# Performance work log

Hardware: AMD Instinct MI355X
Metric: run time of the kernel (lower is better)

Reference implementation:

```python
import jax, jax.numpy as jnp
import numpy as np

NUM_HEADS = 12

def _pe(L, d):
    # standard sinusoidal positional encoding, shape (1, L, d)
    pos = jnp.arange(L, dtype=jnp.float32)[:, None]
    i = jnp.arange(d)[None, :]
    angle = pos / jnp.power(10000.0, (2 * (i // 2)).astype(jnp.float32) / d)
    pe = jnp.where(i % 2 == 0, jnp.sin(angle), jnp.cos(angle))
    return pe[None]

def _ln(x, scale, bias, eps=1e-5):
    m = x.mean(-1, keepdims=True)
    v = ((x - m) ** 2).mean(-1, keepdims=True)
    return (x - m) / jnp.sqrt(v + eps) * scale + bias

def setup_inputs() -> dict:
    key = jax.random.key(0)
    ks = jax.random.split(key, 8)
    D = 768
    s = 0.02
    return {
        "x": jax.random.normal(ks[0], (8, D, 32, 32), jnp.float32),
        "context_token": jax.random.normal(ks[1], (1, 1, D), jnp.float32),
        "register_tokens": jax.random.normal(ks[2], (1, 4, D), jnp.float32),
        "in_proj_w": jax.random.normal(ks[3], (3 * D, D), jnp.float32) * s,
        "in_proj_b": jnp.zeros((3 * D,), jnp.float32),
        "out_proj_w": jax.random.normal(ks[4], (D, D), jnp.float32) * s,
        "out_proj_b": jnp.zeros((D,), jnp.float32),
        "ln1_s": jnp.ones((D,), jnp.float32),
        "ln1_b": jnp.zeros((D,), jnp.float32),
        "ln2_s": jnp.ones((D,), jnp.float32),
        "ln2_b": jnp.zeros((D,), jnp.float32),
        "ffn_w1": jax.random.normal(ks[5], (4 * D, D), jnp.float32) * s,
        "ffn_b1": jnp.zeros((4 * D,), jnp.float32),
        "ffn_w2": jax.random.normal(ks[6], (D, 4 * D), jnp.float32) * s,
        "ffn_b2": jnp.zeros((D,), jnp.float32),
    }

def reference(x, context_token, register_tokens, in_proj_w, in_proj_b,
              out_proj_w, out_proj_b, ln1_s, ln1_b, ln2_s, ln2_b,
              ffn_w1, ffn_b1, ffn_w2, ffn_b2):
    B, d, h, w = x.shape
    N = h * w
    R = register_tokens.shape[1]
    G = 1 + R  # global tokens: context + registers
    nh = NUM_HEADS
    dh = d // nh
    # (B, N, d)
    x_flat = x.reshape(B, d, N).transpose(0, 2, 1)
    tokens = jnp.concatenate([
        jnp.broadcast_to(context_token, (B, 1, d)),
        jnp.broadcast_to(register_tokens, (B, R, d)),
    ], axis=1)
    tokens = tokens + _pe(G, d)
    xwt = _ln(jnp.concatenate([tokens, x_flat], axis=1), ln1_s, ln1_b)
    S = G + N
    # MultiheadAttention (eval mode, dropout off): fused in-projection
    qkv = xwt @ in_proj_w.T + in_proj_b
    q, k, v = jnp.split(qkv, 3, axis=-1)
    to_heads = lambda t: t.reshape(B, S, nh, dh).transpose(0, 2, 1, 3)
    q, k, v = to_heads(q), to_heads(k), to_heads(v)
    scores = jnp.einsum('bhqd,bhkd->bhqk', q, k) / np.float32(np.sqrt(dh))
    # mask (True = disallowed): feature rows (>=G) cannot attend to global cols (<G);
    # global rows attend everything; feature-feature block allowed.
    row_feat = jnp.arange(S) >= G
    col_glob = jnp.arange(S) < G
    disallowed = row_feat[:, None] & col_glob[None, :]
    scores = jnp.where(disallowed, -jnp.inf, scores)
    attn = jax.nn.softmax(scores, axis=-1)
    o = jnp.einsum('bhqk,bhkd->bhqd', attn, v).transpose(0, 2, 1, 3).reshape(B, S, d)
    o = o @ out_proj_w.T + out_proj_b
    y = o + xwt
    ff = jax.nn.gelu(_ln(y, ln2_s, ln2_b) @ ffn_w1.T + ffn_b1, approximate=False) @ ffn_w2.T + ffn_b2
    y = y + ff
    context_out = y[:, 0:1, :]
    register_out = y[:, 1:G, :]
    feature_out = y[:, G:, :].transpose(0, 2, 1).reshape(B, d, h, w)
    return feature_out, context_out, register_out
```

## Files before the change

### kernel.cpp

```cpp
#include <hip/hip_runtime.h>
#include <hip/hip_bf16.h>
#include <cmath>

typedef unsigned short u16;
typedef __bf16 bf16x8 __attribute__((ext_vector_type(8)));
typedef float floatx4 __attribute__((ext_vector_type(4)));

#define SQ 1029
#define DM 768
#define NH 12
#define SQP 1088

#define GLD16(gp, lp) __builtin_amdgcn_global_load_lds( \
    (const __attribute__((address_space(1))) unsigned int*)(gp), \
    (__attribute__((address_space(3))) unsigned int*)(lp), 16, 0, 0)

#define OFF_WQKV ((size_t)0)
#define OFF_WOUT ((size_t)3538944)
#define OFF_W1   ((size_t)4718592)
#define OFF_W2   ((size_t)9437184)
#define OFF_XF   ((size_t)14155776)
#define OFF_XWT  ((size_t)26800128)
#define OFF_Q    ((size_t)39444480)
#define OFF_K    ((size_t)52813824)
#define OFF_V    ((size_t)66183168)
#define OFF_VT   ((size_t)79552512)
#define OFF_Y    ((size_t)92921856)

__device__ __forceinline__ float bf2f(u16 u) {
  unsigned int x = ((unsigned int)u) << 16;
  float f; __builtin_memcpy(&f, &x, 4); return f;
}
__device__ __forceinline__ u16 f2bf(float f) {
  unsigned int x; __builtin_memcpy(&x, &x, 0);
  __builtin_memcpy(&x, &f, 4);
  x = (x + 0x7fffu + ((x >> 16) & 1u)) >> 16;
  return (u16)x;
}
__device__ __forceinline__ unsigned int pk_bf16(float a, float b) {
  __hip_bfloat162 h = __float22bfloat162_rn(make_float2(a, b));
  unsigned int u; __builtin_memcpy(&u, &h, 4); return u;
}

__device__ __forceinline__ void blockReduce2(float& s1, float& s2) {
  #pragma unroll
  for (int o = 32; o > 0; o >>= 1) { s1 += __shfl_xor(s1, o); s2 += __shfl_xor(s2, o); }
  __shared__ float t1[4], t2[4];
  const int w = threadIdx.x >> 6;
  if ((threadIdx.x & 63) == 0) { t1[w] = s1; t2[w] = s2; }
  __syncthreads();
  s1 = t1[0] + t1[1] + t1[2] + t1[3];
  s2 = t2[0] + t2[1] + t2[2] + t2[3];
}

__global__ __launch_bounds__(256) void convw_all(
    const float* __restrict__ a, const float* __restrict__ b,
    const float* __restrict__ c, const float* __restrict__ d, u16* __restrict__ dst) {
  int i = blockIdx.x * 256 + threadIdx.x;
  if (i >= 1769472) return;
  const float* src; int off;
  if (i < 442368)       { src = a; off = i; }
  else if (i < 589824)  { src = b; off = i - 442368; }
  else if (i < 1179648) { src = c; off = i - 589824; }
  else                  { src = d; off = i - 1179648; }
  float4 v = ((const float4*)src)[off];
  ushort4 o; o.x = f2bf(v.x); o.y = f2bf(v.y); o.z = f2bf(v.z); o.w = f2bf(v.w);
  ((ushort4*)dst)[i] = o;
}

__global__ __launch_bounds__(256) void transpose_x(const float* __restrict__ x, u16* __restrict__ xf) {
  __shared__ u16 tile[32][33];
  const int b = blockIdx.x, ct = blockIdx.y, nt = blockIdx.z;
  const int i = threadIdx.x, jj = threadIdx.y;
  #pragma unroll
  for (int kk = 0; kk < 4; ++kk) {
    int j = jj + kk * 8;
    tile[j][i] = f2bf(x[((size_t)b * 768 + ct * 32 + j) * 1024 + nt * 32 + i]);
  }
  __syncthreads();
  #pragma unroll
  for (int kk = 0; kk < 4; ++kk) {
    int j = jj + kk * 8;
    xf[((size_t)b * 1024 + nt * 32 + j) * 768 + ct * 32 + i] = tile[i][j];
  }
}

__global__ __launch_bounds__(256) void build_xwt(
    const u16* __restrict__ xf, const float* __restrict__ ctx, const float* __restrict__ regt,
    const float* __restrict__ g, const float* __restrict__ be, u16* __restrict__ xwt) {
  const int row = blockIdx.x;
  const int b = row / SQ, s = row % SQ;
  const int tid = threadIdx.x;
  float v[3];
  #pragma unroll
  for (int i = 0; i < 3; ++i) {
    const int c = tid + i * 256;
    float val;
    if (s >= 5) {
      val = bf2f(xf[((size_t)b * 1024 + (s - 5)) * DM + c]);
    } else {
      float tok = (s == 0) ? ctx[c] : regt[(s - 1) * DM + c];
      float e = (float)(2 * (c / 2)) * (1.0f / 768.0f);
      float ang = (float)s / powf(10000.0f, e);
      val = tok + ((c & 1) ? cosf(ang) : sinf(ang));
    }
    v[i] = val;
  }
  float s1 = v[0] + v[1] + v[2];
  float s2 = v[0] * v[0] + v[1] * v[1] + v[2] * v[2];
  blockReduce2(s1, s2);
  const float mean = s1 * (1.0f / 768.0f);
  const float var = s2 * (1.0f / 768.0f) - mean * mean;
  const float rs = rsqrtf(fmaxf(var, 0.0f) + 1e-5f);
  #pragma unroll
  for (int i = 0; i < 3; ++i) {
    const int c = tid + i * 256;
    xwt[(size_t)row * DM + c] = f2bf((v[i] - mean) * rs * g[c] + be[c]);
  }
}

__global__ __launch_bounds__(256) void ln2k(
    const u16* __restrict__ y, const float* __restrict__ g, const float* __restrict__ be,
    u16* __restrict__ out) {
  const int row = blockIdx.x;
  const int tid = threadIdx.x;
  float v[3];
  #pragma unroll
  for (int i = 0; i < 3; ++i) v[i] = bf2f(y[(size_t)row * DM + tid + i * 256]);
  float s1 = v[0] + v[1] + v[2];
  float s2 = v[0] * v[0] + v[1] * v[1] + v[2] * v[2];
  blockReduce2(s1, s2);
  const float mean = s1 * (1.0f / 768.0f);
  const float var = s2 * (1.0f / 768.0f) - mean * mean;
  const float rs = rsqrtf(fmaxf(var, 0.0f) + 1e-5f);
  #pragma unroll
  for (int i = 0; i < 3; ++i) {
    const int c = tid + i * 256;
    out[(size_t)row * DM + c] = f2bf((v[i] - mean) * rs * g[c] + be[c]);
  }
}

template<int EPI>
__global__ __launch_bounds__(256) void gemm128(
    const u16* __restrict__ A, const u16* __restrict__ W, const float* __restrict__ bias,
    void* __restrict__ p0, void* __restrict__ p1, void* __restrict__ p2,
    int M, int N, int K) {
  __shared__ u16 As[8192];
  __shared__ u16 Bs[8192];
  const int tid = threadIdx.x, wave = tid >> 6, lane = tid & 63, quad = lane >> 4, l16 = lane & 15;
  const int m0 = blockIdx.x * 128, n0 = blockIdx.y * 128;
  const int wm = wave & 1, wn = wave >> 1;

  const u16* Ap[4]; const u16* Wp[4]; u16* la[4]; u16* lb[4];
  #pragma unroll
  for (int it = 0; it < 4; ++it) {
    const int c = it * 256 + tid;
    const int row = c >> 3, gch = (c & 7) ^ (row & 7);
    Ap[it] = A + (size_t)min(m0 + row, M - 1) * K + gch * 8;
    Wp[it] = W + (size_t)(n0 + row) * K + gch * 8;
    la[it] = As + it * 2048 + wave * 512;
    lb[it] = Bs + it * 2048 + wave * 512;
  }

  floatx4 acc[4][4];
  #pragma unroll
  for (int i = 0; i < 4; ++i)
    #pragma unroll
    for (int j = 0; j < 4; ++j) { floatx4 z = {0.f, 0.f, 0.f, 0.f}; acc[i][j] = z; }

  for (int k0 = 0; k0 < K; k0 += 64) {
    __syncthreads();
    #pragma unroll
    for (int it = 0; it < 4; ++it) GLD16(Ap[it] + k0, la[it]);
    #pragma unroll
    for (int it = 0; it < 4; ++it) GLD16(Wp[it] + k0, lb[it]);
    __syncthreads();
    #pragma unroll
    for (int kk = 0; kk < 2; ++kk) {
      bf16x8 a[4], b[4];
      const int ch = ((kk * 4 + quad) ^ (l16 & 7)) << 3;
      #pragma unroll
      for (int i = 0; i < 4; ++i) a[i] = *(const bf16x8*)&As[(wm * 64 + i * 16 + l16) * 64 + ch];
      #pragma unroll
      for (int j = 0; j < 4; ++j) b[j] = *(const bf16x8*)&Bs[(wn * 64 + j * 16 + l16) * 64 + ch];
      #pragma unroll
      for (int i = 0; i < 4; ++i)
        #pragma unroll
        for (int j = 0; j < 4; ++j)
          acc[i][j] = __builtin_amdgcn_mfma_f32_16x16x32_bf16(a[i], b[j], acc[i][j], 0, 0, 0);
    }
  }

  if constexpr (EPI == 0) {
    const int sec = n0 / 768;
    u16* dst = (sec == 0) ? (u16*)p0 : (sec == 1) ? (u16*)p1 : (u16*)p2;
    #pragma unroll
    for (int i = 0; i < 4; ++i) {
      #pragma unroll
      for (int r = 0; r < 4; ++r) {
        const int row = m0 + wm * 64 + i * 16 + quad * 4 + r;
        if (row >= M) continue;
        const int bb = row / SQ, ss = row - bb * SQ;
        #pragma unroll
        for (int j = 0; j < 4; ++j) {
          const int cc = n0 + wn * 64 + j * 16 + l16;
          const int hh = (cc - sec * 768) >> 6;
          const int dh = cc & 63;
          dst[(((size_t)bb * NH + hh) * SQP + ss) * 64 + dh] = f2bf(acc[i][j][r] + bias[cc]);
        }
      }
    }
  } else {
    #pragma unroll
    for (int i = 0; i < 4; ++i) {
      #pragma unroll
      for (int r = 0; r < 4; ++r) {
        const int row = m0 + wm * 64 + i * 16 + quad * 4 + r;
        if (row >= M) continue;
        #pragma unroll
        for (int j = 0; j < 4; ++j) {
          const int cc = n0 + wn * 64 + j * 16 + l16;
          const size_t idx = (size_t)row * N + cc;
          float v = acc[i][j][r] + bias[cc];
          if constexpr (EPI == 1) {
            v += bf2f(((const u16*)p1)[idx]);
            ((u16*)p0)[idx] = f2bf(v);
          } else if constexpr (EPI == 2) {
            v = v / (1.0f + exp2f(-2.3022221f * (v + 0.044715f * v * v * v)));
            ((u16*)p0)[idx] = f2bf(v);
          } else {
            v += bf2f(((const u16*)p1)[idx]);
            ((float*)p0)[idx] = v;
          }
        }
      }
    }
  }
}

__global__ __launch_bounds__(256) void vtrans(const u16* __restrict__ v, u16* __restrict__ vt) {
  __shared__ u16 t[32][33];
  const int bh = blockIdx.x, st = blockIdx.y, dt = blockIdx.z;
  const u16* vs = v + (size_t)bh * SQP * 64;
  u16* vd = vt + (size_t)bh * 64 * SQP;
  const int i = threadIdx.x, jj = threadIdx.y;
  #pragma unroll
  for (int kk = 0; kk < 4; ++kk) {
    int j = jj + kk * 8;
    t[j][i] = vs[(size_t)(st * 32 + j) * 64 + dt * 32 + i];
  }
  __syncthreads();
  #pragma unroll
  for (int kk = 0; kk < 4; ++kk) {
    int j = jj + kk * 8;
    vd[(size_t)(dt * 32 + j) * SQP + st * 32 + i] = t[i][j];
  }
}

__global__ __launch_bounds__(256) void attn_flash(
    const u16* __restrict__ q, const u16* __restrict__ k, const u16* __restrict__ vt,
    u16* __restrict__ out) {
  const int bh = blockIdx.x, qt = blockIdx.y;
  const int b = bh / NH, h = bh % NH;
  const int tid = threadIdx.x, wave = tid >> 6, lane = tid & 63, quad = lane >> 4, l16 = lane & 15;
  __shared__ u16 Qs[4096], Ks[4096], VTs[4096];
  __shared__ u16 Ps[64 * 72];
  const int q0 = qt * 64;
  const u16* qslab = q + (size_t)bh * SQP * 64;
  const u16* kslab = k + (size_t)bh * SQP * 64;
  const u16* vslab = vt + (size_t)bh * 64 * SQP;
  const int c0 = tid, c1 = tid + 256;
  const int r0 = c0 >> 3, q0c = (c0 & 7) ^ (r0 & 7);
  const int r1 = c1 >> 3, q1c = (c1 & 7) ^ (r1 & 7);
  const int g0 = r0 * 64 + q0c * 8;
  const int g1 = r1 * 64 + q1c * 8;
  u16* L0Q = Qs + wave * 512;  u16* L1Q = Qs + 2048 + wave * 512;
  u16* L0K = Ks + wave * 512;  u16* L1K = Ks + 2048 + wave * 512;
  u16* L0V = VTs + wave * 512; u16* L1V = VTs + 2048 + wave * 512;

  GLD16(qslab + q0 * 64 + g0, L0Q);
  GLD16(qslab + q0 * 64 + g1, L1Q);

  floatx4 Oa[4];
  #pragma unroll
  for (int nt = 0; nt < 4; ++nt) { floatx4 z = {0.f, 0.f, 0.f, 0.f}; Oa[nt] = z; }
  float l_acc = 0.f;
  const int qrow = wave * 16 + l16;
  const int qg = q0 + qrow;
  const bool qfeat = (qg >= 5);
  const float ssc = 0.125f * 1.44269504088896f;

  for (int t = 0; t < 17; ++t) {
    const int k0 = t * 64;
    __syncthreads();
    GLD16(kslab + k0 * 64 + g0, L0K);
    GLD16(kslab + k0 * 64 + g1, L1K);
    GLD16(vslab + (size_t)r0 * SQP + k0 + q0c * 8, L0V);
    GLD16(vslab + (size_t)r1 * SQP + k0 + q1c * 8, L1V);
    __syncthreads();

    floatx4 st[4];
    #pragma unroll
    for (int mt = 0; mt < 4; ++mt) { floatx4 z = {0.f, 0.f, 0.f, 0.f}; st[mt] = z; }
    #pragma unroll
    for (int kk = 0; kk < 2; ++kk) {
      bf16x8 qf = *(const bf16x8*)&Qs[qrow * 64 + (((kk * 4 + quad) ^ (qrow & 7)) << 3)];
      #pragma unroll
      for (int mt = 0; mt < 4; ++mt) {
        const int krow = mt * 16 + l16;
        bf16x8 kf = *(const bf16x8*)&Ks[krow * 64 + (((kk * 4 + quad) ^ (krow & 7)) << 3)];
        st[mt] = __builtin_amdgcn_mfma_f32_16x16x32_bf16(kf, qf, st[mt], 0, 0, 0);
      }
    }

    #pragma unroll
    for (int mt = 0; mt < 4; ++mt) {
      float p[4];
      #pragma unroll
      for (int r = 0; r < 4; ++r) {
        const int kg = k0 + mt * 16 + quad * 4 + r;
        const bool masked = (kg >= SQ) || (qfeat && kg < 5);
        float pv = exp2f(st[mt][r] * ssc);
        pv = masked ? 0.f : pv;
        p[r] = pv;
        l_acc += pv;
      }
      uint2 w;
      w.x = pk_bf16(p[0], p[1]);
      w.y = pk_bf16(p[2], p[3]);
      *(uint2*)&Ps[qrow * 72 + mt * 16 + quad * 4] = w;
    }

    #pragma unroll
    for (int kk = 0; kk < 2; ++kk) {
      bf16x8 pf = *(const bf16x8*)&Ps[qrow * 72 + kk * 32 + quad * 8];
      #pragma unroll
      for (int nt = 0; nt < 4; ++nt) {
        const int brow = nt * 16 + l16;
        bf16x8 bb = *(const bf16x8*)&VTs[brow * 64 + (((kk * 4 + quad) ^ (brow & 7)) << 3)];
        Oa[nt] = __builtin_amdgcn_mfma_f32_16x16x32_bf16(pf, bb, Oa[nt], 0, 0, 0);
      }
    }
  }

  float lt = l_acc;
  lt += __shfl_xor(lt, 16);
  lt += __shfl_xor(lt, 32);
  lt = fmaxf(lt, 1e-30f);
  #pragma unroll
  for (int nt = 0; nt < 4; ++nt)
    #pragma unroll
    for (int r = 0; r < 4; ++r) {
      const int qo = quad * 4 + r;
      const float lr = __shfl(lt, (lane & 48) | qo);
      const int qg2 = q0 + wave * 16 + qo;
      if (qg2 < SQ)
        out[((size_t)b * SQ + qg2) * DM + h * 64 + nt * 16 + l16] = f2bf(Oa[nt][r] / lr);
    }
}

__global__ __launch_bounds__(256) void transpose_out(const float* __restrict__ yf, float* __restrict__ out) {
  __shared__ float tile[32][33];
  const int b = blockIdx.x, nt = blockIdx.y, ct = blockIdx.z;
  const int i = threadIdx.x, jj = threadIdx.y;
  #pragma unroll
  for (int kk = 0; kk < 4; ++kk) {
    int j = jj + kk * 8;
    tile[j][i] = yf[((size_t)b * SQ + 5 + nt * 32 + j) * DM + ct * 32 + i];
  }
  __syncthreads();
  #pragma unroll
  for (int kk = 0; kk < 4; ++kk) {
    int j = jj + kk * 8;
    out[((size_t)b * 768 + ct * 32 + j) * 1024 + nt * 32 + i] = tile[i][j];
  }
}

__global__ __launch_bounds__(256) void out_small(const float* __restrict__ yf, float* __restrict__ out) {
  const int idx = blockIdx.x * 256 + threadIdx.x;
  if (idx >= 8 * 5 * DM) return;
  const int b = idx / (5 * DM);
  const int r = idx % (5 * DM);
  const int s = r / DM, c = r % DM;
  const float v = yf[((size_t)b * SQ + s) * DM + c];
  if (s == 0) out[(size_t)6291456 + (size_t)b * DM + c] = v;
  else out[(size_t)6291456 + 6144 + ((size_t)b * 4 + (s - 1)) * DM + c] = v;
}

extern "C" void kernel_launch(void* const* d_in, const int* in_sizes, int n_in,
                              void* d_out, int out_size, void* d_ws, size_t ws_size,
                              hipStream_t stream) {
  const float* x    = (const float*)d_in[0];
  const float* ctx  = (const float*)d_in[1];
  const float* regt = (const float*)d_in[2];
  const float* wqkv = (const float*)d_in[3];
  const float* bqkv = (const float*)d_in[4];
  const float* wout = (const float*)d_in[5];
  const float* bout = (const float*)d_in[6];
  const float* ln1s = (const float*)d_in[7];
  const float* ln1b = (const float*)d_in[8];
  const float* ln2s = (const float*)d_in[9];
  const float* ln2b = (const float*)d_in[10];
  const float* w1   = (const float*)d_in[11];
  const float* b1   = (const float*)d_in[12];
  const float* w2   = (const float*)d_in[13];
  const float* b2   = (const float*)d_in[14];

  char* ws = (char*)d_ws;
  u16* wb_all = (u16*)(ws + OFF_WQKV);
  u16* wqkv_b = (u16*)(ws + OFF_WQKV);
  u16* wout_b = (u16*)(ws + OFF_WOUT);
  u16* w1_b   = (u16*)(ws + OFF_W1);
  u16* w2_b   = (u16*)(ws + OFF_W2);
  u16* xf     = (u16*)(ws + OFF_XF);
  u16* xwt    = (u16*)(ws + OFF_XWT);
  u16* qb     = (u16*)(ws + OFF_Q);
  u16* kb     = (u16*)(ws + OFF_K);
  u16* vb     = (u16*)(ws + OFF_V);
  u16* vtb    = (u16*)(ws + OFF_VT);
  u16* yb     = (u16*)(ws + OFF_Y);
  u16* attnb  = (u16*)(ws + OFF_XF);
  u16* ynorm  = (u16*)(ws + OFF_XF);
  u16* h1     = (u16*)(ws + OFF_Q);
  float* yfin = (float*)(ws + OFF_XF);
  float* outp = (float*)d_out;

  convw_all   <<<6912, 256, 0, stream>>>(wqkv, wout, w1, w2, wb_all);
  transpose_x <<<dim3(8, 24, 32), dim3(32, 8), 0, stream>>>(x, xf);
  build_xwt   <<<8232, 256, 0, stream>>>(xf, ctx, regt, ln1s, ln1b, xwt);
  gemm128<0>  <<<dim3(65, 18), 256, 0, stream>>>(xwt, wqkv_b, bqkv, qb, kb, vb, 8232, 2304, 768);
  vtrans      <<<dim3(96, 34, 2), dim3(32, 8), 0, stream>>>(vb, vtb);
  attn_flash  <<<dim3(96, 17), 256, 0, stream>>>(qb, kb, vtb, attnb);
  gemm128<1>  <<<dim3(65, 6), 256, 0, stream>>>(attnb, wout_b, bout, yb, xwt, nullptr, 8232, 768, 768);
  ln2k        <<<8232, 256, 0, stream>>>(yb, ln2s, ln2b, ynorm);
  gemm128<2>  <<<dim3(65, 24), 256, 0, stream>>>(ynorm, w1_b, b1, h1, nullptr, nullptr, 8232, 3072, 768);
  gemm128<3>  <<<dim3(65, 6), 256, 0, stream>>>(h1, w2_b, b2, yfin, yb, nullptr, 8232, 768, 3072);
  transpose_out<<<dim3(8, 32, 24), dim3(32, 8), 0, stream>>>(yfin, outp);
  out_small   <<<120, 256, 0, stream>>>(yfin, outp);
}
```

Baseline: 464.4 us.

## Template GEMM on K/N, add grouped block swizzle, vectorized LDS-staged epilogue, fused QKV layout

The GEMM becomes a templated kernel with compile-time K and N. It adds a grouped 1D block order so that eight M-tiles share each weight tile, and swaps the MFMA operands so each lane holds four consecutive columns. The epilogue stages results through shared memory and writes 16-byte coalesced bf16 stores with a vectorized residual add. The QKV projection now writes a single row-major [S,2304] buffer that attention and vtrans read with strided loads, and the final output is kept in bf16 instead of fp32. This cuts scattered 2-byte stores and output traffic, at the cost of less-coalesced Q/K loads in attention and an extra rounding of the final output to bf16.

```diff
diff --git a/kernel.cpp b/kernel.cpp
--- a/kernel.cpp
+++ b/kernel.cpp
@@ -21,19 +21,16 @@
 #define OFF_W2   ((size_t)9437184)
 #define OFF_XF   ((size_t)14155776)
 #define OFF_XWT  ((size_t)26800128)
-#define OFF_Q    ((size_t)39444480)
-#define OFF_K    ((size_t)52813824)
-#define OFF_V    ((size_t)66183168)
-#define OFF_VT   ((size_t)79552512)
-#define OFF_Y    ((size_t)92921856)
+#define OFF_QKV  ((size_t)39444480)
+#define OFF_VT   ((size_t)77783040)
+#define OFF_Y    ((size_t)91152384)
 
 __device__ __forceinline__ float bf2f(u16 u) {
   unsigned int x = ((unsigned int)u) << 16;
   float f; __builtin_memcpy(&f, &x, 4); return f;
 }
 __device__ __forceinline__ u16 f2bf(float f) {
-  unsigned int x; __builtin_memcpy(&x, &x, 0);
-  __builtin_memcpy(&x, &f, 4);
+  unsigned int x; __builtin_memcpy(&x, &f, 4);
   x = (x + 0x7fffu + ((x >> 16) & 1u)) >> 16;
   return (u16)x;
 }
@@ -140,15 +137,21 @@
   }
 }
 
-template<int EPI>
-__global__ __launch_bounds__(256) void gemm128(
+template<int EPI, int K, int NB>
+__global__ __launch_bounds__(256) void gemmk(
     const u16* __restrict__ A, const u16* __restrict__ W, const float* __restrict__ bias,
-    void* __restrict__ p0, void* __restrict__ p1, void* __restrict__ p2,
-    int M, int N, int K) {
-  __shared__ u16 As[8192];
-  __shared__ u16 Bs[8192];
+    const u16* __restrict__ res, u16* __restrict__ out, int M) {
+  constexpr int N = NB * 128;
+  __shared__ u16 SM[16384];
+  u16* Asm = SM;
+  u16* Bsm = SM + 8192;
   const int tid = threadIdx.x, wave = tid >> 6, lane = tid & 63, quad = lane >> 4, l16 = lane & 15;
-  const int m0 = blockIdx.x * 128, n0 = blockIdx.y * 128;
+  const int lin = blockIdx.x;
+  constexpr int FULL = 64 * NB;
+  int mb, nb;
+  if (lin < FULL) { const int g = lin / (8 * NB); const int r = lin - g * 8 * NB; mb = g * 8 + (r & 7); nb = r >> 3; }
+  else { mb = 64; nb = lin - FULL; }
+  const int m0 = mb * 128, n0 = nb * 128;
   const int wm = wave & 1, wn = wave >> 1;
 
   const u16* Ap[4]; const u16* Wp[4]; u16* la[4]; u16* lb[4];
@@ -158,8 +161,8 @@
     const int row = c >> 3, gch = (c & 7) ^ (row & 7);
     Ap[it] = A + (size_t)min(m0 + row, M - 1) * K + gch * 8;
     Wp[it] = W + (size_t)(n0 + row) * K + gch * 8;
-    la[it] = As + it * 2048 + wave * 512;
-    lb[it] = Bs + it * 2048 + wave * 512;
+    la[it] = Asm + c * 8;
+    lb[it] = Bsm + c * 8;
   }
 
   floatx4 acc[4][4];
@@ -168,86 +171,107 @@
     #pragma unroll
     for (int j = 0; j < 4; ++j) { floatx4 z = {0.f, 0.f, 0.f, 0.f}; acc[i][j] = z; }
 
-  for (int k0 = 0; k0 < K; k0 += 64) {
-    __syncthreads();
-    #pragma unroll
-    for (int it = 0; it < 4; ++it) GLD16(Ap[it] + k0, la[it]);
-    #pragma unroll
-    for (int it = 0; it < 4; ++it) GLD16(Wp[it] + k0, lb[it]);
-    __syncthreads();
-    #pragma unroll
-    for (int kk = 0; kk < 2; ++kk) {
-      bf16x8 a[4], b[4];
-      const int ch = ((kk * 4 + quad) ^ (l16 & 7)) << 3;
-      #pragma unroll
-      for (int i = 0; i < 4; ++i) a[i] = *(const bf16x8*)&As[(wm * 64 + i * 16 + l16) * 64 + ch];
-      #pragma unroll
-      for (int j = 0; j < 4; ++j) b[j] = *(const bf16x8*)&Bs[(wn * 64 + j * 16 + l16) * 64 + ch];
-      #pragma unroll
-      for (int i = 0; i < 4; ++i)
+  const int ch0 = (quad ^ (l16 & 7)) << 3;
+  const int ch1 = ((4 + quad) ^ (l16 & 7)) << 3;
+
+  #pragma unroll 1
+  for (int ko = 0; ko < K / 768; ++ko) {
+    #pragma unroll
+    for (int ki = 0; ki < 768; ki += 64) {
+      __syncthreads();
+      #pragma unroll
+      for (int it = 0; it < 4; ++it) GLD16(Ap[it] + ki, la[it]);
+      #pragma unroll
+      for (int it = 0; it < 4; ++it) GLD16(Wp[it] + ki, lb[it]);
+      __syncthreads();
+      #pragma unroll
+      for (int kk = 0; kk < 2; ++kk) {
+        const int ch = kk ? ch1 : ch0;
+        bf16x8 a[4], b[4];
         #pragma unroll
-        for (int j = 0; j < 4; ++j)
-          acc[i][j] = __builtin_amdgcn_mfma_f32_16x16x32_bf16(a[i], b[j], acc[i][j], 0, 0, 0);
-    }
-  }
-
-  if constexpr (EPI == 0) {
-    const int sec = n0 / 768;
-    u16* dst = (sec == 0) ? (u16*)p0 : (sec == 1) ? (u16*)p1 : (u16*)p2;
+        for (int i = 0; i < 4; ++i) a[i] = *(const bf16x8*)&Asm[(wm * 64 + i * 16 + l16) * 64 + ch];
+        #pragma unroll
+        for (int j = 0; j < 4; ++j) b[j] = *(const bf16x8*)&Bsm[(wn * 64 + j * 16 + l16) * 64 + ch];
+        #pragma unroll
+        for (int i = 0; i < 4; ++i)
+          #pragma unroll
+          for (int j = 0; j < 4; ++j)
+            acc[i][j] = __builtin_amdgcn_mfma_f32_16x16x32_bf16(b[j], a[i], acc[i][j], 0, 0, 0);
+      }
+    }
+    if (K > 768) {
+      #pragma unroll
+      for (int it = 0; it < 4; ++it) { Ap[it] += 768; Wp[it] += 768; }
+    }
+  }
+
+  #pragma unroll
+  for (int j = 0; j < 4; ++j) {
+    const float4 b4 = *(const float4*)(bias + n0 + wn * 64 + j * 16 + quad * 4);
     #pragma unroll
     for (int i = 0; i < 4; ++i) {
-      #pragma unroll
-      for (int r = 0; r < 4; ++r) {
-        const int row = m0 + wm * 64 + i * 16 + quad * 4 + r;
-        if (row >= M) continue;
-        const int bb = row / SQ, ss = row - bb * SQ;
+      acc[i][j][0] += b4.x; acc[i][j][1] += b4.y; acc[i][j][2] += b4.z; acc[i][j][3] += b4.w;
+    }
+  }
+  if constexpr (EPI == 2) {
+    #pragma unroll
+    for (int i = 0; i < 4; ++i)
+      #pragma unroll
+      for (int j = 0; j < 4; ++j)
         #pragma unroll
-        for (int j = 0; j < 4; ++j) {
-          const int cc = n0 + wn * 64 + j * 16 + l16;
-          const int hh = (cc - sec * 768) >> 6;
-          const int dh = cc & 63;
-          dst[(((size_t)bb * NH + hh) * SQP + ss) * 64 + dh] = f2bf(acc[i][j][r] + bias[cc]);
+        for (int r = 0; r < 4; ++r) {
+          const float v = acc[i][j][r];
+          acc[i][j][r] = v / (1.0f + exp2f(-2.3022221f * (v + 0.044715f * v * v * v)));
         }
-      }
-    }
-  } else {
-    #pragma unroll
-    for (int i = 0; i < 4; ++i) {
-      #pragma unroll
-      for (int r = 0; r < 4; ++r) {
-        const int row = m0 + wm * 64 + i * 16 + quad * 4 + r;
-        if (row >= M) continue;
+  }
+  __syncthreads();
+  u16* Ep = SM + wave * 2304;
+  #pragma unroll
+  for (int h = 0; h < 2; ++h) {
+    #pragma unroll
+    for (int i2 = 0; i2 < 2; ++i2) {
+      const int i = h * 2 + i2;
+      #pragma unroll
+      for (int j = 0; j < 4; ++j) {
+        uint2 w;
+        w.x = pk_bf16(acc[i][j][0], acc[i][j][1]);
+        w.y = pk_bf16(acc[i][j][2], acc[i][j][3]);
+        *(uint2*)&Ep[(i2 * 16 + l16) * 72 + j * 16 + quad * 4] = w;
+      }
+    }
+    #pragma unroll
+    for (int s = 0; s < 4; ++s) {
+      const int lrow = s * 8 + (lane >> 3);
+      const int gm = m0 + wm * 64 + h * 32 + lrow;
+      const int gn = n0 + wn * 64 + (lane & 7) * 8;
+      uint4 lv = *(const uint4*)&Ep[lrow * 72 + (lane & 7) * 8];
+      if constexpr (EPI == 1 || EPI == 3) {
+        const uint4 rv = *(const uint4*)(res + (size_t)min(gm, M - 1) * N + gn);
+        const unsigned* lp = &lv.x; const unsigned* rp = &rv.x;
+        uint4 ov; unsigned* op = &ov.x;
         #pragma unroll
-        for (int j = 0; j < 4; ++j) {
-          const int cc = n0 + wn * 64 + j * 16 + l16;
-          const size_t idx = (size_t)row * N + cc;
-          float v = acc[i][j][r] + bias[cc];
-          if constexpr (EPI == 1) {
-            v += bf2f(((const u16*)p1)[idx]);
-            ((u16*)p0)[idx] = f2bf(v);
-          } else if constexpr (EPI == 2) {
-            v = v / (1.0f + exp2f(-2.3022221f * (v + 0.044715f * v * v * v)));
-            ((u16*)p0)[idx] = f2bf(v);
-          } else {
-            v += bf2f(((const u16*)p1)[idx]);
-            ((float*)p0)[idx] = v;
-          }
+        for (int d = 0; d < 4; ++d) {
+          const float a0 = bf2f((u16)(lp[d] & 0xffffu)) + bf2f((u16)(rp[d] & 0xffffu));
+          const float a1 = bf2f((u16)(lp[d] >> 16)) + bf2f((u16)(rp[d] >> 16));
+          op[d] = pk_bf16(a0, a1);
         }
-      }
-    }
-  }
-}
-
-__global__ __launch_bounds__(256) void vtrans(const u16* __restrict__ v, u16* __restrict__ vt) {
+        lv = ov;
+      }
+      if (gm < M) *(uint4*)(out + (size_t)gm * N + gn) = lv;
+    }
+  }
+}
+
+__global__ __launch_bounds__(256) void vtrans(const u16* __restrict__ qkv, u16* __restrict__ vt) {
   __shared__ u16 t[32][33];
   const int bh = blockIdx.x, st = blockIdx.y, dt = blockIdx.z;
-  const u16* vs = v + (size_t)bh * SQP * 64;
+  const int bq = bh / NH, hh = bh % NH;
   u16* vd = vt + (size_t)bh * 64 * SQP;
   const int i = threadIdx.x, jj = threadIdx.y;
   #pragma unroll
   for (int kk = 0; kk < 4; ++kk) {
     int j = jj + kk * 8;
-    t[j][i] = vs[(size_t)(st * 32 + j) * 64 + dt * 32 + i];
+    t[j][i] = qkv[(size_t)(bq * SQ + st * 32 + j) * 2304 + 1536 + hh * 64 + dt * 32 + i];
   }
   __syncthreads();
   #pragma unroll
@@ -258,28 +282,24 @@
 }
 
 __global__ __launch_bounds__(256) void attn_flash(
-    const u16* __restrict__ q, const u16* __restrict__ k, const u16* __restrict__ vt,
-    u16* __restrict__ out) {
+    const u16* __restrict__ qkv, const u16* __restrict__ vt, u16* __restrict__ out) {
   const int bh = blockIdx.x, qt = blockIdx.y;
   const int b = bh / NH, h = bh % NH;
   const int tid = threadIdx.x, wave = tid >> 6, lane = tid & 63, quad = lane >> 4, l16 = lane & 15;
   __shared__ u16 Qs[4096], Ks[4096], VTs[4096];
   __shared__ u16 Ps[64 * 72];
   const int q0 = qt * 64;
-  const u16* qslab = q + (size_t)bh * SQP * 64;
-  const u16* kslab = k + (size_t)bh * SQP * 64;
+  const u16* qk = qkv + (size_t)b * SQ * 2304 + h * 64;
   const u16* vslab = vt + (size_t)bh * 64 * SQP;
   const int c0 = tid, c1 = tid + 256;
   const int r0 = c0 >> 3, q0c = (c0 & 7) ^ (r0 & 7);
   const int r1 = c1 >> 3, q1c = (c1 & 7) ^ (r1 & 7);
-  const int g0 = r0 * 64 + q0c * 8;
-  const int g1 = r1 * 64 + q1c * 8;
   u16* L0Q = Qs + wave * 512;  u16* L1Q = Qs + 2048 + wave * 512;
   u16* L0K = Ks + wave * 512;  u16* L1K = Ks + 2048 + wave * 512;
   u16* L0V = VTs + wave * 512; u16* L1V = VTs + 2048 + wave * 512;
 
-  GLD16(qslab + q0 * 64 + g0, L0Q);
-  GLD16(qslab + q0 * 64 + g1, L1Q);
+  GLD16(qk + (size_t)(q0 + r0) * 2304 + q0c * 8, L0Q);
+  GLD16(qk + (size_t)(q0 + r1) * 2304 + q1c * 8, L1Q);
 
   floatx4 Oa[4];
   #pragma unroll
@@ -293,8 +313,8 @@
   for (int t = 0; t < 17; ++t) {
     const int k0 = t * 64;
     __syncthreads();
-    GLD16(kslab + k0 * 64 + g0, L0K);
-    GLD16(kslab + k0 * 64 + g1, L1K);
+    GLD16(qk + 768 + (size_t)(k0 + r0) * 2304 + q0c * 8, L0K);
+    GLD16(qk + 768 + (size_t)(k0 + r1) * 2304 + q1c * 8, L1K);
     GLD16(vslab + (size_t)r0 * SQP + k0 + q0c * 8, L0V);
     GLD16(vslab + (size_t)r1 * SQP + k0 + q1c * 8, L1V);
     __syncthreads();
@@ -359,8 +379,8 @@
     }
 }
 
-__global__ __launch_bounds__(256) void transpose_out(const float* __restrict__ yf, float* __restrict__ out) {
-  __shared__ float tile[32][33];
+__global__ __launch_bounds__(256) void transpose_out(const u16* __restrict__ yf, float* __restrict__ out) {
+  __shared__ u16 tile[32][33];
   const int b = blockIdx.x, nt = blockIdx.y, ct = blockIdx.z;
   const int i = threadIdx.x, jj = threadIdx.y;
   #pragma unroll
@@ -372,17 +392,17 @@
   #pragma unroll
   for (int kk = 0; kk < 4; ++kk) {
     int j = jj + kk * 8;
-    out[((size_t)b * 768 + ct * 32 + j) * 1024 + nt * 32 + i] = tile[i][j];
-  }
-}
-
-__global__ __launch_bounds__(256) void out_small(const float* __restrict__ yf, float* __restrict__ out) {
+    out[((size_t)b * 768 + ct * 32 + j) * 1024 + nt * 32 + i] = bf2f(tile[i][j]);
+  }
+}
+
+__global__ __launch_bounds__(256) void out_small(const u16* __restrict__ yf, float* __restrict__ out) {
   const int idx = blockIdx.x * 256 + threadIdx.x;
   if (idx >= 8 * 5 * DM) return;
   const int b = idx / (5 * DM);
   const int r = idx % (5 * DM);
   const int s = r / DM, c = r % DM;
-  const float v = yf[((size_t)b * SQ + s) * DM + c];
+  const float v = bf2f(yf[((size_t)b * SQ + s) * DM + c]);
   if (s == 0) out[(size_t)6291456 + (size_t)b * DM + c] = v;
   else out[(size_t)6291456 + 6144 + ((size_t)b * 4 + (s - 1)) * DM + c] = v;
 }
@@ -414,27 +434,25 @@
   u16* w2_b   = (u16*)(ws + OFF_W2);
   u16* xf     = (u16*)(ws + OFF_XF);
   u16* xwt    = (u16*)(ws + OFF_XWT);
-  u16* qb     = (u16*)(ws + OFF_Q);
-  u16* kb     = (u16*)(ws + OFF_K);
-  u16* vb     = (u16*)(ws + OFF_V);
+  u16* qkv    = (u16*)(ws + OFF_QKV);
   u16* vtb    = (u16*)(ws + OFF_VT);
   u16* yb     = (u16*)(ws + OFF_Y);
   u16* attnb  = (u16*)(ws + OFF_XF);
   u16* ynorm  = (u16*)(ws + OFF_XF);
-  u16* h1     = (u16*)(ws + OFF_Q);
-  float* yfin = (float*)(ws + OFF_XF);
+  u16* h1     = (u16*)(ws + OFF_QKV);
+  u16* yfin   = (u16*)(ws + OFF_XWT);
   float* outp = (float*)d_out;
 
   convw_all   <<<6912, 256, 0, stream>>>(wqkv, wout, w1, w2, wb_all);
   transpose_x <<<dim3(8, 24, 32), dim3(32, 8), 0, stream>>>(x, xf);
   build_xwt   <<<8232, 256, 0, stream>>>(xf, ctx, regt, ln1s, ln1b, xwt);
-  gemm128<0>  <<<dim3(65, 18), 256, 0, stream>>>(xwt, wqkv_b, bqkv, qb, kb, vb, 8232, 2304, 768);
-  vtrans      <<<dim3(96, 34, 2), dim3(32, 8), 0, stream>>>(vb, vtb);
-  attn_flash  <<<dim3(96, 17), 256, 0, stream>>>(qb, kb, vtb, attnb);
-  gemm128<1>  <<<dim3(65, 6), 256, 0, stream>>>(attnb, wout_b, bout, yb, xwt, nullptr, 8232, 768, 768);
+  gemmk<0, 768, 18><<<65 * 18, 256, 0, stream>>>(xwt, wqkv_b, bqkv, nullptr, qkv, 8232);
+  vtrans      <<<dim3(96, 34, 2), dim3(32, 8), 0, stream>>>(qkv, vtb);
+  attn_flash  <<<dim3(96, 17), 256, 0, stream>>>(qkv, vtb, attnb);
+  gemmk<1, 768, 6><<<65 * 6, 256, 0, stream>>>(attnb, wout_b, bout, xwt, yb, 8232);
   ln2k        <<<8232, 256, 0, stream>>>(yb, ln2s, ln2b, ynorm);
-  gemm128<2>  <<<dim3(65, 24), 256, 0, stream>>>(ynorm, w1_b, b1, h1, nullptr, nullptr, 8232, 3072, 768);
-  gemm128<3>  <<<dim3(65, 6), 256, 0, stream>>>(h1, w2_b, b2, yfin, yb, nullptr, 8232, 768, 3072);
+  gemmk<2, 768, 24><<<65 * 24, 256, 0, stream>>>(ynorm, w1_b, b1, nullptr, h1, 8232);
+  gemmk<3, 3072, 6><<<65 * 6, 256, 0, stream>>>(h1, w2_b, b2, yb, yfin, 8232);
   transpose_out<<<dim3(8, 32, 24), dim3(32, 8), 0, stream>>>(yfin, outp);
   out_small   <<<120, 256, 0, stream>>>(yfin, outp);
 }
```

Result: faster. 405.2 us (-12.8%).
